# Kernel optimization log

Measured on AMD Instinct MI355X. Metric: run time of the kernel, lower is better.

## Reference

```python
import jax, jax.numpy as jnp
import numpy as np

IN_CH = 64
KEY_CH = 4
HEADS = 4
VAL_CH = 32


def setup_inputs() -> dict:
    key = jax.random.key(0)
    ks = jax.random.split(key, 9)
    def w(k, shape, fan_in):
        b = 1.0 / np.sqrt(fan_in)
        return jax.random.uniform(k, shape, jnp.float32, -b, b)
    return {
        "input_": jax.random.normal(ks[0], (4, IN_CH, 64, 64, 64), jnp.float32),
        "Wk": w(ks[1], (KEY_CH, IN_CH), IN_CH),
        "bk": w(ks[2], (KEY_CH,), IN_CH),
        "Wq": w(ks[3], (KEY_CH, IN_CH), IN_CH),
        "bq": w(ks[4], (KEY_CH,), IN_CH),
        "Wv": w(ks[5], (VAL_CH, IN_CH), IN_CH),
        "bv": w(ks[6], (VAL_CH,), IN_CH),
        "Wr": w(ks[7], (IN_CH, VAL_CH), VAL_CH),
        "br": w(ks[8], (IN_CH,), VAL_CH),
    }


def reference(input_, Wk, bk, Wq, bq, Wv, bv, Wr, br):
    n, c, h, w_, l = input_.shape
    N = h * w_ * l
    x = input_.reshape(n, c, N)  # 1x1 Conv3d == pointwise linear over channels
    keys = jnp.einsum('kc,bcn->bkn', Wk, x) + bk[None, :, None]
    queries = jnp.einsum('kc,bcn->bkn', Wq, x) + bq[None, :, None]
    values = jnp.einsum('vc,bcn->bvn', Wv, x) + bv[None, :, None]
    hk = KEY_CH // HEADS   # 1
    hv = VAL_CH // HEADS   # 8
    k = jax.nn.softmax(keys.reshape(n, HEADS, hk, N), axis=3)       # softmax over tokens
    q = jax.nn.softmax(queries.reshape(n, HEADS, hk, N), axis=2)    # softmax over head channels
    v = values.reshape(n, HEADS, hv, N)
    # context: (b,H,hk,hv); attended: (b,H,hv,N)
    context = jnp.einsum('bhkn,bhvn->bhkv', k, v)
    attended = jnp.einsum('bhkv,bhkn->bhvn', context, q)
    agg = attended.reshape(n, VAL_CH, N)
    reproj = jnp.einsum('cv,bvn->bcn', Wr, agg) + br[None, :, None]
    return (reproj + x).reshape(n, c, h, w_, l)
```

## Files before the change

kernel.cpp:

```cpp
#include <hip/hip_runtime.h>

#define NTOK 262144
#define NCH  64
#define NB   4

#define TPB   512
#define TILE  256
#define GRIDX 64
#define NIT   (NTOK / (GRIDX * TILE))

#define WS_S  0
#define WS_M  16
#define WS_RC 1040

typedef float floatx4 __attribute__((ext_vector_type(4)));
typedef const __attribute__((address_space(1))) unsigned int* gas1p;
typedef __attribute__((address_space(3))) unsigned int*       las3p;

__global__ __launch_bounds__(TPB)
void ea3d_reduce(const float* __restrict__ x, const float* __restrict__ Wk,
                 float* __restrict__ ws)
{
    __shared__ __align__(16) float buf[2][NCH][TILE];
    __shared__ __align__(16) float es[TILE][4];
    __shared__ __align__(16) float wk4[NCH][4];
    __shared__ float ssum[8][4];

    const int tid = threadIdx.x;
    const int w   = tid >> 6;
    const int l   = tid & 63;
    const int b   = blockIdx.y;

    if (tid < 256) wk4[tid >> 2][tid & 3] = Wk[(tid & 3) * NCH + (tid >> 2)];
    __syncthreads();

    const float* xb = x + (size_t)b * NCH * NTOK;
    const size_t tokblk = (size_t)blockIdx.x * (TILE * NIT);
    const int    c0 = w << 3;

    float macc[32];
    #pragma unroll
    for (int r = 0; r < 32; ++r) macc[r] = 0.f;
    float sacc[4] = {0.f, 0.f, 0.f, 0.f};

    auto stage = [&](int tt) {
        const size_t t0 = tokblk + (size_t)tt * TILE + (l << 2);
        float* dbase = &buf[tt & 1][c0][0];
        #pragma unroll
        for (int i = 0; i < 8; ++i) {
            const float* src = xb + (size_t)(c0 + i) * NTOK + t0;
            float* dst = dbase + i * TILE;
            __builtin_amdgcn_global_load_lds((gas1p)src, (las3p)dst, 16, 0, 0);
        }
    };

    stage(0);

    #pragma unroll 1
    for (int t = 0; t < NIT; ++t) {
        asm volatile("s_waitcnt vmcnt(0)" ::: "memory");
        __builtin_amdgcn_s_barrier();
        asm volatile("" ::: "memory");

        if (t + 1 < NIT) stage(t + 1);

        const float* bt = &buf[t & 1][0][0];
        const int tk  = (w << 5) + (l & 31);
        const int ch0 = (l >> 5) << 5;
        float k0 = 0.f, k1 = 0.f, k2 = 0.f, k3 = 0.f;
        #pragma unroll
        for (int j = 0; j < 32; ++j) {
            float  xv = bt[(ch0 + j) * TILE + tk];
            float4 wv = *(const float4*)&wk4[ch0 + j][0];
            k0 += wv.x * xv; k1 += wv.y * xv; k2 += wv.z * xv; k3 += wv.w * xv;
        }
        k0 += __shfl_xor(k0, 32); k1 += __shfl_xor(k1, 32);
        k2 += __shfl_xor(k2, 32); k3 += __shfl_xor(k3, 32);
        float e0 = __expf(k0), e1 = __expf(k1), e2 = __expf(k2), e3 = __expf(k3);
        if (l < 32) {
            *(float4*)&es[tk][0] = make_float4(e0, e1, e2, e3);
            sacc[0] += e0; sacc[1] += e1; sacc[2] += e2; sacc[3] += e3;
        }

        asm volatile("s_waitcnt lgkmcnt(0)" ::: "memory");
        __builtin_amdgcn_s_barrier();
        asm volatile("" ::: "memory");

        const int t4 = l << 2;
        float4 ea = *(const float4*)&es[t4 + 0][0];
        float4 eb = *(const float4*)&es[t4 + 1][0];
        float4 ec = *(const float4*)&es[t4 + 2][0];
        float4 ed = *(const float4*)&es[t4 + 3][0];
        #pragma unroll
        for (int i = 0; i < 8; ++i) {
            float4 xv = *(const float4*)&buf[t & 1][c0 + i][t4];
            macc[i*4+0] += ea.x*xv.x + eb.x*xv.y + ec.x*xv.z + ed.x*xv.w;
            macc[i*4+1] += ea.y*xv.x + eb.y*xv.y + ec.y*xv.z + ed.y*xv.w;
            macc[i*4+2] += ea.z*xv.x + eb.z*xv.y + ec.z*xv.z + ed.z*xv.w;
            macc[i*4+3] += ea.w*xv.x + eb.w*xv.y + ec.w*xv.z + ed.w*xv.w;
        }
    }

    #pragma unroll
    for (int r = 0; r < 32; ++r) {
        float v = macc[r];
        v += __shfl_xor(v, 1);  v += __shfl_xor(v, 2);
        v += __shfl_xor(v, 4);  v += __shfl_xor(v, 8);
        v += __shfl_xor(v, 16); v += __shfl_xor(v, 32);
        macc[r] = v;
    }
    if (l == 0) {
        float* mb = ws + WS_M + (size_t)(b * 4) * NCH + c0;
        #pragma unroll
        for (int i = 0; i < 8; ++i) {
            #pragma unroll
            for (int h = 0; h < 4; ++h)
                __hip_atomic_fetch_add(mb + h * NCH + i, macc[i*4+h],
                                       __ATOMIC_RELAXED, __HIP_MEMORY_SCOPE_AGENT);
        }
    }

    {
        float v0 = sacc[0], v1 = sacc[1], v2 = sacc[2], v3 = sacc[3];
        #pragma unroll
        for (int off = 1; off < 32; off <<= 1) {
            v0 += __shfl_xor(v0, off); v1 += __shfl_xor(v1, off);
            v2 += __shfl_xor(v2, off); v3 += __shfl_xor(v3, off);
        }
        if (l == 0) { ssum[w][0] = v0; ssum[w][1] = v1; ssum[w][2] = v2; ssum[w][3] = v3; }
    }
    __syncthreads();
    if (tid < 4) {
        float s = 0.f;
        #pragma unroll
        for (int w2 = 0; w2 < 8; ++w2) s += ssum[w2][tid];
        __hip_atomic_fetch_add(ws + WS_S + b * 4 + tid, s,
                               __ATOMIC_RELAXED, __HIP_MEMORY_SCOPE_AGENT);
    }
}

__global__ void ea3d_finalize(const float* __restrict__ Wv, const float* __restrict__ bv,
                              const float* __restrict__ Wr, const float* __restrict__ br,
                              float* __restrict__ ws)
{
    __shared__ float ctx[NB * 32];
    const int tid = threadIdx.x;
    if (tid < 128) {
        int b = tid >> 5, hv = tid & 31, h = hv >> 3;
        float inv = 1.0f / ws[WS_S + b * 4 + h];
        const float* m = ws + WS_M + (b * 4 + h) * NCH;
        const float* wvr = Wv + hv * NCH;
        float acc = 0.f;
        #pragma unroll
        for (int c = 0; c < NCH; ++c) acc += wvr[c] * m[c];
        ctx[b * 32 + hv] = acc * inv + bv[hv];
    }
    __syncthreads();
    int b = tid >> 6, c = tid & 63;
    const float* wrr = Wr + c * 32;
    const float* cb  = ctx + b * 32;
    float acc = br[c];
    #pragma unroll
    for (int hv = 0; hv < 32; ++hv) acc += wrr[hv] * cb[hv];
    ws[WS_RC + b * NCH + c] = acc;
}

__global__ __launch_bounds__(256)
void ea3d_add(const float* __restrict__ x, const float* __restrict__ ws,
              float* __restrict__ out)
{
    const int row = blockIdx.y;
    const float rc = ws[WS_RC + row];
    const size_t base = (size_t)row * NTOK;
    const float4*  xp = (const float4*)(x + base);
    floatx4*       op = (floatx4*)(out + base);
    const int nvec = NTOK / 4;
    for (int i = blockIdx.x * blockDim.x + threadIdx.x; i < nvec;
         i += gridDim.x * blockDim.x) {
        float4 v = xp[i];
        floatx4 nv = { v.x + rc, v.y + rc, v.z + rc, v.w + rc };
        __builtin_nontemporal_store(nv, op + i);
    }
}

extern "C" void kernel_launch(void* const* d_in, const int* in_sizes, int n_in,
                              void* d_out, int out_size, void* d_ws, size_t ws_size,
                              hipStream_t stream)
{
    const float* x  = (const float*)d_in[0];
    const float* Wk = (const float*)d_in[1];
    const float* Wv = (const float*)d_in[5];
    const float* bv = (const float*)d_in[6];
    const float* Wr = (const float*)d_in[7];
    const float* br = (const float*)d_in[8];
    float* out = (float*)d_out;
    float* ws  = (float*)d_ws;

    (void)hipMemsetAsync(ws, 0, WS_RC * sizeof(float), stream);
    ea3d_reduce<<<dim3(GRIDX, NB), TPB, 0, stream>>>(x, Wk, ws);
    ea3d_finalize<<<1, 256, 0, stream>>>(Wv, bv, Wr, br, ws);
    ea3d_add<<<dim3(32, NB * NCH), 256, 0, stream>>>(x, ws, out);
}
```

Measured before the change: 165.7 us.

## Single-buffer larger token tile and compute keys one token per thread

Doubles the token tile to 512 and drops the LDS double buffer, so the next tile is staged only after the current one is fully consumed. Each thread now computes all 64 channels of the key projection for one token, with no cross-lane shuffle, and writes exp values to a padded per-head LDS array. The context accumulation reads scalar values per token instead of float4 groups. This halves the loop iteration count and simplifies the key step, but it removes the overlap between global loads and compute and adds a third barrier per iteration.

New measurement: 164.7 us, median of 2. Within noise of the previous version (-0.6%).

```diff
diff --git a/kernel.cpp b/kernel.cpp
--- a/kernel.cpp
+++ b/kernel.cpp
@@ -5,7 +5,7 @@
 #define NB   4
 
 #define TPB   512
-#define TILE  256
+#define TILE  512
 #define GRIDX 64
 #define NIT   (NTOK / (GRIDX * TILE))
 
@@ -21,8 +21,8 @@
 void ea3d_reduce(const float* __restrict__ x, const float* __restrict__ Wk,
                  float* __restrict__ ws)
 {
-    __shared__ __align__(16) float buf[2][NCH][TILE];
-    __shared__ __align__(16) float es[TILE][4];
+    __shared__ __align__(16) float buf[NCH][TILE];
+    __shared__ __align__(16) float es2[4][TILE + 8];
     __shared__ __align__(16) float wk4[NCH][4];
     __shared__ float ssum[8][4];
 
@@ -45,12 +45,11 @@
 
     auto stage = [&](int tt) {
         const size_t t0 = tokblk + (size_t)tt * TILE + (l << 2);
-        float* dbase = &buf[tt & 1][c0][0];
         #pragma unroll
         for (int i = 0; i < 8; ++i) {
             const float* src = xb + (size_t)(c0 + i) * NTOK + t0;
-            float* dst = dbase + i * TILE;
-            __builtin_amdgcn_global_load_lds((gas1p)src, (las3p)dst, 16, 0, 0);
+            __builtin_amdgcn_global_load_lds((gas1p)src,         (las3p)&buf[c0 + i][0],   16, 0, 0);
+            __builtin_amdgcn_global_load_lds((gas1p)(src + 256), (las3p)&buf[c0 + i][256], 16, 0, 0);
         }
     };
 
@@ -62,23 +61,17 @@
         __builtin_amdgcn_s_barrier();
         asm volatile("" ::: "memory");
 
-        if (t + 1 < NIT) stage(t + 1);
-
-        const float* bt = &buf[t & 1][0][0];
-        const int tk  = (w << 5) + (l & 31);
-        const int ch0 = (l >> 5) << 5;
-        float k0 = 0.f, k1 = 0.f, k2 = 0.f, k3 = 0.f;
-        #pragma unroll
-        for (int j = 0; j < 32; ++j) {
-            float  xv = bt[(ch0 + j) * TILE + tk];
-            float4 wv = *(const float4*)&wk4[ch0 + j][0];
-            k0 += wv.x * xv; k1 += wv.y * xv; k2 += wv.z * xv; k3 += wv.w * xv;
-        }
-        k0 += __shfl_xor(k0, 32); k1 += __shfl_xor(k1, 32);
-        k2 += __shfl_xor(k2, 32); k3 += __shfl_xor(k3, 32);
-        float e0 = __expf(k0), e1 = __expf(k1), e2 = __expf(k2), e3 = __expf(k3);
-        if (l < 32) {
-            *(float4*)&es[tk][0] = make_float4(e0, e1, e2, e3);
+        {
+            const int tk = tid;
+            float k0 = 0.f, k1 = 0.f, k2 = 0.f, k3 = 0.f;
+            #pragma unroll 16
+            for (int c = 0; c < NCH; ++c) {
+                float  xv = buf[c][tk];
+                float4 wv = *(const float4*)&wk4[c][0];
+                k0 += wv.x * xv; k1 += wv.y * xv; k2 += wv.z * xv; k3 += wv.w * xv;
+            }
+            float e0 = __expf(k0), e1 = __expf(k1), e2 = __expf(k2), e3 = __expf(k3);
+            es2[0][tk] = e0; es2[1][tk] = e1; es2[2][tk] = e2; es2[3][tk] = e3;
             sacc[0] += e0; sacc[1] += e1; sacc[2] += e2; sacc[3] += e3;
         }
 
@@ -86,19 +79,25 @@
         __builtin_amdgcn_s_barrier();
         asm volatile("" ::: "memory");
 
-        const int t4 = l << 2;
-        float4 ea = *(const float4*)&es[t4 + 0][0];
-        float4 eb = *(const float4*)&es[t4 + 1][0];
-        float4 ec = *(const float4*)&es[t4 + 2][0];
-        float4 ed = *(const float4*)&es[t4 + 3][0];
-        #pragma unroll
-        for (int i = 0; i < 8; ++i) {
-            float4 xv = *(const float4*)&buf[t & 1][c0 + i][t4];
-            macc[i*4+0] += ea.x*xv.x + eb.x*xv.y + ec.x*xv.z + ed.x*xv.w;
-            macc[i*4+1] += ea.y*xv.x + eb.y*xv.y + ec.y*xv.z + ed.y*xv.w;
-            macc[i*4+2] += ea.z*xv.x + eb.z*xv.y + ec.z*xv.z + ed.z*xv.w;
-            macc[i*4+3] += ea.w*xv.x + eb.w*xv.y + ec.w*xv.z + ed.w*xv.w;
-        }
+        #pragma unroll
+        for (int s = 0; s < 8; ++s) {
+            const int tk = l + (s << 6);
+            float e0 = es2[0][tk], e1 = es2[1][tk], e2 = es2[2][tk], e3 = es2[3][tk];
+            #pragma unroll
+            for (int i = 0; i < 8; ++i) {
+                float xv = buf[c0 + i][tk];
+                macc[i*4+0] += e0 * xv;
+                macc[i*4+1] += e1 * xv;
+                macc[i*4+2] += e2 * xv;
+                macc[i*4+3] += e3 * xv;
+            }
+        }
+
+        asm volatile("s_waitcnt lgkmcnt(0)" ::: "memory");
+        __builtin_amdgcn_s_barrier();
+        asm volatile("" ::: "memory");
+
+        if (t + 1 < NIT) stage(t + 1);
     }
 
     #pragma unroll
@@ -123,7 +122,7 @@
     {
         float v0 = sacc[0], v1 = sacc[1], v2 = sacc[2], v3 = sacc[3];
         #pragma unroll
-        for (int off = 1; off < 32; off <<= 1) {
+        for (int off = 1; off < 64; off <<= 1) {
             v0 += __shfl_xor(v0, off); v1 += __shfl_xor(v1, off);
             v2 += __shfl_xor(v2, off); v3 += __shfl_xor(v3, off);
         }
```
